# Kernel optimization log

Measured on AMD Instinct MI355X. Metric: run time of the kernel, lower is better.

The kernel has to match this reference:

```python
import jax, jax.numpy as jnp
import numpy as np

TOP_K = 8


def setup_inputs() -> dict:
    key = jax.random.key(0)
    ks = jax.random.split(key, 5)
    B, S, H, E, I = 2, 1024, 2048, 64, 768
    return {
        "hidden_states": jax.random.normal(ks[0], (B, S, H), dtype=jnp.float32),
        "router_w": jax.random.normal(ks[1], (H, E), dtype=jnp.float32) * 0.02,
        "gate_w": jax.random.normal(ks[2], (E, H, I), dtype=jnp.float32) * 0.02,
        "up_w": jax.random.normal(ks[3], (E, H, I), dtype=jnp.float32) * 0.02,
        "down_w": jax.random.normal(ks[4], (E, I, H), dtype=jnp.float32) * 0.02,
    }


def reference(hidden_states, router_w, gate_w, up_w, down_w):
    B, S, H = hidden_states.shape
    E = router_w.shape[1]
    x = hidden_states.reshape(-1, H)                      # [T, H]
    T = x.shape[0]

    router_logits = x @ router_w                           # [T, E]
    probs = jax.nn.softmax(router_logits.astype(jnp.float32), axis=-1)
    topk_w, topk_idx = jax.lax.top_k(probs, TOP_K)         # [T, K]
    topk_w = topk_w / jnp.sum(topk_w, axis=-1, keepdims=True)  # norm_topk_prob
    topk_w = topk_w.astype(x.dtype)

    # Dense combine weights: zero for non-selected experts -> same math as the
    # gather/scatter loop, jit-friendly (no data-dependent shapes).
    combine = jnp.zeros((T, E), dtype=x.dtype)
    combine = combine.at[jnp.arange(T)[:, None], topk_idx].set(topk_w)  # [T, E]

    g = jnp.einsum('th,ehi->tei', x, gate_w)               # [T, E, I]
    u = jnp.einsum('th,ehi->tei', x, up_w)                 # [T, E, I]
    h = jax.nn.silu(g) * u                                 # SwiGLU
    out = jnp.einsum('te,tei,eih->th', combine, h, down_w)  # weighted combine

    return out.reshape(B, S, H), router_logits
```

## Files before the change

kernel.cpp:

```cpp
#include <hip/hip_runtime.h>
#include <hip/hip_bf16.h>

typedef __hip_bfloat16 bf16;
typedef short s16x8 __attribute__((ext_vector_type(8)));
typedef unsigned short u16x8 __attribute__((ext_vector_type(8)));
typedef float f32x4 __attribute__((ext_vector_type(4)));

#define T_TOK 2048
#define HDIM  2048
#define NEXP  64
#define IDIM  768
#define TOPK  8
#define OUT_OFF (T_TOK * HDIM)
#define NPAIR (T_TOK * TOPK)

#define WS_TOPK_IDX  0
#define WS_TOPK_W    (64 * 1024)
#define WS_PAIR_TOK  (128 * 1024)
#define WS_SLOT_OF   (192 * 1024)
#define WS_COUNTS    (256 * 1024)
#define WS_OFFSETS   (257 * 1024)
#define WS_CURSOR    (258 * 1024)
#define WS_H         (1024 * 1024)
#define WS_PARTIAL   (WS_H + (size_t)NPAIR * IDIM * 2)
#define WS_XB        WS_PARTIAL

__device__ __forceinline__ float bf_to_f(unsigned short u) {
    return __uint_as_float(((unsigned int)u) << 16);
}
__device__ __forceinline__ unsigned short f2bf(float f) {
    unsigned int u = __float_as_uint(f);
    unsigned int r = (u + 0x7FFFu + ((u >> 16) & 1u)) >> 16;
    return (unsigned short)r;
}
__device__ __forceinline__ unsigned cvtpk(float lo, float hi) {
    unsigned r;
    asm("v_cvt_pk_bf16_f32 %0, %1, %2" : "=v"(r) : "v"(lo), "v"(hi));
    return r;
}

typedef const __attribute__((address_space(1))) unsigned int* gas_ptr;
typedef __attribute__((address_space(3))) unsigned int* las_ptr;
__device__ __forceinline__ void gload_lds16(const void* g, void* l) {
    __builtin_amdgcn_global_load_lds((gas_ptr)g, (las_ptr)l, 16, 0, 0);
}

__global__ __launch_bounds__(256) void xbf_kernel(const float* __restrict__ x,
                                                  unsigned short* __restrict__ xb) {
    int i = blockIdx.x * 256 + threadIdx.x;
    const float4* src = (const float4*)x + (size_t)i * 2;
    float4 a = src[0], b = src[1];
    u16x8 o;
    o[0] = f2bf(a.x); o[1] = f2bf(a.y); o[2] = f2bf(a.z); o[3] = f2bf(a.w);
    o[4] = f2bf(b.x); o[5] = f2bf(b.y); o[6] = f2bf(b.z); o[7] = f2bf(b.w);
    ((u16x8*)xb)[i] = o;
}

__global__ __launch_bounds__(256) void router_kernel(
    const float* __restrict__ x, const float* __restrict__ rw,
    float* __restrict__ logits) {
    int wave = threadIdx.x >> 6;
    int lane = threadIdx.x & 63;
    int t = blockIdx.x * 4 + wave;
    const float4* x4 = (const float4*)(x + (size_t)t * HDIM);
    float acc = 0.f;
    for (int h4 = 0; h4 < HDIM / 4; ++h4) {
        float4 xv = x4[h4];
        int h = h4 * 4;
        acc = fmaf(xv.x, rw[(h + 0) * NEXP + lane], acc);
        acc = fmaf(xv.y, rw[(h + 1) * NEXP + lane], acc);
        acc = fmaf(xv.z, rw[(h + 2) * NEXP + lane], acc);
        acc = fmaf(xv.w, rw[(h + 3) * NEXP + lane], acc);
    }
    logits[t * NEXP + lane] = acc;
}

__global__ __launch_bounds__(64) void topk_kernel(
    const float* __restrict__ logits, int* __restrict__ topk_idx,
    float* __restrict__ topk_w, int* __restrict__ counts) {
    int t = blockIdx.x;
    int lane = threadIdx.x;
    float lg = logits[t * NEXP + lane];
    float mx = lg;
    for (int off = 32; off; off >>= 1) mx = fmaxf(mx, __shfl_xor(mx, off));
    float ex = expf(lg - mx);
    float sum = ex;
    for (int off = 32; off; off >>= 1) sum += __shfl_xor(sum, off);
    float prob = ex / sum;

    float pr = prob;
    float myv = 0.f;
    int myidx = 0;
    float ksum = 0.f;
    for (int k = 0; k < TOPK; ++k) {
        float v = pr;
        int idx = lane;
        for (int off = 32; off; off >>= 1) {
            float ov = __shfl_xor(v, off);
            int oi = __shfl_xor(idx, off);
            if (ov > v || (ov == v && oi < idx)) { v = ov; idx = oi; }
        }
        ksum += v;
        if (lane == k) { myidx = idx; myv = v; }
        if (lane == idx) pr = -1.f;
    }
    if (lane < TOPK) {
        topk_idx[t * TOPK + lane] = myidx;
        topk_w[t * TOPK + lane] = myv / ksum;
        atomicAdd(&counts[myidx], 1);
    }
}

__global__ __launch_bounds__(64) void scan_kernel(
    const int* __restrict__ counts, int* __restrict__ offsets, int* __restrict__ cursor) {
    int lane = threadIdx.x;
    int c = counts[lane];
    int incl = c;
    for (int off = 1; off < 64; off <<= 1) {
        int tt = __shfl_up(incl, off);
        if (lane >= off) incl += tt;
    }
    offsets[lane] = incl - c;
    if (lane == 63) offsets[64] = incl;
    cursor[lane] = 0;
}

__global__ __launch_bounds__(256) void scatter_kernel(
    const int* __restrict__ topk_idx, const int* __restrict__ offsets,
    int* __restrict__ cursor, int* __restrict__ pair_token, int* __restrict__ slot_of) {
    int i = blockIdx.x * 256 + threadIdx.x;
    if (i >= NPAIR) return;
    int t = i >> 3;
    int e = topk_idx[i];
    int pos = atomicAdd(&cursor[e], 1);
    int slot = offsets[e] + pos;
    pair_token[slot] = t;
    slot_of[i] = slot;
}

#define BM   128
#define BKS  64
#define LDP  72

__global__ __launch_bounds__(256) void gateup_mfma(
    const unsigned short* __restrict__ xb, const float* __restrict__ gate_w,
    const float* __restrict__ up_w, const int* __restrict__ offsets,
    const int* __restrict__ pair_token, unsigned short* __restrict__ hbuf) {
    int e = blockIdx.x;
    int ntile = blockIdx.z;
    int off = offsets[e];
    int cnt = offsets[e + 1] - off;
    if (cnt <= 0) return;

    __shared__ unsigned short As[2][BM * BKS];
    __shared__ unsigned short Bg[2][64 * LDP];
    __shared__ unsigned short Bu[2][64 * LDP];
    __shared__ int toks[BM];

    int tid = threadIdx.x;
    int lane = tid & 63;
    int wave = tid >> 6;
    int wr = wave >> 1, wc = wave & 1;
    int l15 = lane & 15, lg4 = lane >> 4;

    int nI = tid & 15, kQ = tid >> 4;
    int n4 = nI * 4, kB = kQ * 4;
    const float* gcol = gate_w + (size_t)e * HDIM * IDIM + ntile * 64 + (size_t)kB * IDIM + n4;
    const float* ucol = up_w   + (size_t)e * HDIM * IDIM + ntile * 64 + (size_t)kB * IDIM + n4;

    for (int mt = blockIdx.y; mt * BM < cnt; mt += gridDim.y) {
        int m0 = mt * BM;
        if (tid < BM) {
            int p = m0 + tid;
            toks[tid] = pair_token[off + (p < cnt ? p : 0)];
        }
        __syncthreads();
        const unsigned short* aq[4];
        #pragma unroll
        for (int q = 0; q < 4; ++q) {
            int mloc = q * 32 + wave * 8 + (lane >> 3);
            int j2 = (lane & 7) ^ (mloc & 7);
            aq[q] = xb + (size_t)toks[mloc] * HDIM + j2 * 8;
        }
        f32x4 accg[4][2] = {};
        f32x4 accu[4][2] = {};

        #pragma unroll
        for (int q = 0; q < 4; ++q)
            gload_lds16(aq[q], &As[0][(q * 256 + wave * 64) * 8]);
        float4 G[4], U[4];
        #pragma unroll
        for (int i = 0; i < 4; ++i) {
            G[i] = *(const float4*)(gcol + (size_t)i * IDIM);
            U[i] = *(const float4*)(ucol + (size_t)i * IDIM);
        }

        for (int ks = 0; ks < HDIM / BKS; ++ks) {
            int p = ks & 1;
            #pragma unroll
            for (int j = 0; j < 4; ++j) {
                uint2 wg, wu;
                wg.x = cvtpk(((float*)&G[0])[j], ((float*)&G[1])[j]);
                wg.y = cvtpk(((float*)&G[2])[j], ((float*)&G[3])[j]);
                wu.x = cvtpk(((float*)&U[0])[j], ((float*)&U[1])[j]);
                wu.y = cvtpk(((float*)&U[2])[j], ((float*)&U[3])[j]);
                *(uint2*)&Bg[p][(n4 + j) * LDP + kB] = wg;
                *(uint2*)&Bu[p][(n4 + j) * LDP + kB] = wu;
            }
            __syncthreads();
            if (ks + 1 < HDIM / BKS) {
                int h1 = (ks + 1) * BKS;
                #pragma unroll
                for (int q = 0; q < 4; ++q)
                    gload_lds16(aq[q] + h1, &As[p ^ 1][(q * 256 + wave * 64) * 8]);
                #pragma unroll
                for (int i = 0; i < 4; ++i) {
                    G[i] = *(const float4*)(gcol + (size_t)(h1 + i) * IDIM);
                    U[i] = *(const float4*)(ucol + (size_t)(h1 + i) * IDIM);
                }
            }
            #pragma unroll
            for (int kk = 0; kk < 2; ++kk) {
                int krow = kk * 32 + lg4 * 8;
                int jk = kk * 4 + lg4;
                s16x8 a[4], bg2[2], bu2[2];
                #pragma unroll
                for (int mr = 0; mr < 4; ++mr) {
                    int r = wr * 64 + mr * 16 + l15;
                    a[mr] = *(const s16x8*)&As[p][r * 64 + ((jk ^ (r & 7)) * 8)];
                }
                #pragma unroll
                for (int nr = 0; nr < 2; ++nr) {
                    int row = wc * 32 + nr * 16 + l15;
                    bg2[nr] = *(const s16x8*)&Bg[p][row * LDP + krow];
                    bu2[nr] = *(const s16x8*)&Bu[p][row * LDP + krow];
                }
                #pragma unroll
                for (int mr = 0; mr < 4; ++mr)
                    #pragma unroll
                    for (int nr = 0; nr < 2; ++nr) {
                        accg[mr][nr] = __builtin_amdgcn_mfma_f32_16x16x32_bf16(
                            a[mr], bg2[nr], accg[mr][nr], 0, 0, 0);
                        accu[mr][nr] = __builtin_amdgcn_mfma_f32_16x16x32_bf16(
                            a[mr], bu2[nr], accu[mr][nr], 0, 0, 0);
                    }
            }
        }

        #pragma unroll
        for (int mr = 0; mr < 4; ++mr)
            #pragma unroll
            for (int nr = 0; nr < 2; ++nr) {
                int col = ntile * 64 + wc * 32 + nr * 16 + l15;
                #pragma unroll
                for (int reg = 0; reg < 4; ++reg) {
                    int r = m0 + wr * 64 + mr * 16 + lg4 * 4 + reg;
                    if (r < cnt) {
                        float g = accg[mr][nr][reg];
                        float u = accu[mr][nr][reg];
                        float hv = (g / (1.f + __expf(-g))) * u;
                        hbuf[(size_t)(off + r) * IDIM + col] = f2bf(hv);
                    }
                }
            }
    }
}

__global__ __launch_bounds__(256) void down_mfma(
    const unsigned short* __restrict__ hbuf, const float* __restrict__ down_w,
    const int* __restrict__ offsets, unsigned short* __restrict__ partial) {
    int e = blockIdx.x;
    int ntile = blockIdx.z;
    int off = offsets[e];
    int cnt = offsets[e + 1] - off;
    if (cnt <= 0) return;

    __shared__ unsigned short As[2][BM * BKS];
    __shared__ unsigned short Bd[2][128 * LDP];

    int tid = threadIdx.x;
    int lane = tid & 63;
    int wave = tid >> 6;
    int wr = wave >> 1, wc = wave & 1;
    int l15 = lane & 15, lg4 = lane >> 4;

    int nI = tid & 31, kQ0 = tid >> 5;
    int n4 = nI * 4;
    const float* dcol = down_w + (size_t)e * IDIM * HDIM + ntile * 128 + n4;

    for (int mt = blockIdx.y; mt * BM < cnt; mt += gridDim.y) {
        int m0 = mt * BM;
        const unsigned short* aq[4];
        #pragma unroll
        for (int q = 0; q < 4; ++q) {
            int mloc = q * 32 + wave * 8 + (lane >> 3);
            int row = m0 + mloc;
            if (row >= cnt) row = cnt - 1;
            int j2 = (lane & 7) ^ (mloc & 7);
            aq[q] = hbuf + (size_t)(off + row) * IDIM + j2 * 8;
        }
        f32x4 acc[4][4] = {};

        #pragma unroll
        for (int q = 0; q < 4; ++q)
            gload_lds16(aq[q], &As[0][(q * 256 + wave * 64) * 8]);
        float4 D0[4], D1[4];
        #pragma unroll
        for (int i = 0; i < 4; ++i) {
            D0[i] = *(const float4*)(dcol + (size_t)(kQ0 * 4 + i) * HDIM);
            D1[i] = *(const float4*)(dcol + (size_t)((kQ0 + 8) * 4 + i) * HDIM);
        }

        for (int ks = 0; ks < IDIM / BKS; ++ks) {
            int p = ks & 1;
            #pragma unroll
            for (int j = 0; j < 4; ++j) {
                uint2 w0, w1;
                w0.x = cvtpk(((float*)&D0[0])[j], ((float*)&D0[1])[j]);
                w0.y = cvtpk(((float*)&D0[2])[j], ((float*)&D0[3])[j]);
                w1.x = cvtpk(((float*)&D1[0])[j], ((float*)&D1[1])[j]);
                w1.y = cvtpk(((float*)&D1[2])[j], ((float*)&D1[3])[j]);
                *(uint2*)&Bd[p][(n4 + j) * LDP + kQ0 * 4] = w0;
                *(uint2*)&Bd[p][(n4 + j) * LDP + (kQ0 + 8) * 4] = w1;
            }
            __syncthreads();
            if (ks + 1 < IDIM / BKS) {
                int k1 = (ks + 1) * BKS;
                #pragma unroll
                for (int q = 0; q < 4; ++q)
                    gload_lds16(aq[q] + k1, &As[p ^ 1][(q * 256 + wave * 64) * 8]);
                #pragma unroll
                for (int i = 0; i < 4; ++i) {
                    D0[i] = *(const float4*)(dcol + (size_t)(k1 + kQ0 * 4 + i) * HDIM);
                    D1[i] = *(const float4*)(dcol + (size_t)(k1 + (kQ0 + 8) * 4 + i) * HDIM);
                }
            }
            #pragma unroll
            for (int kk = 0; kk < 2; ++kk) {
                int krow = kk * 32 + lg4 * 8;
                int jk = kk * 4 + lg4;
                s16x8 a[4], b[4];
                #pragma unroll
                for (int mr = 0; mr < 4; ++mr) {
                    int r = wr * 64 + mr * 16 + l15;
                    a[mr] = *(const s16x8*)&As[p][r * 64 + ((jk ^ (r & 7)) * 8)];
                }
                #pragma unroll
                for (int nr = 0; nr < 4; ++nr) {
                    int row = wc * 64 + nr * 16 + l15;
                    b[nr] = *(const s16x8*)&Bd[p][row * LDP + krow];
                }
                #pragma unroll
                for (int mr = 0; mr < 4; ++mr)
                    #pragma unroll
                    for (int nr = 0; nr < 4; ++nr)
                        acc[mr][nr] = __builtin_amdgcn_mfma_f32_16x16x32_bf16(
                            a[mr], b[nr], acc[mr][nr], 0, 0, 0);
            }
        }

        #pragma unroll
        for (int mr = 0; mr < 4; ++mr)
            #pragma unroll
            for (int nr = 0; nr < 4; ++nr) {
                int col = ntile * 128 + wc * 64 + nr * 16 + l15;
                #pragma unroll
                for (int reg = 0; reg < 4; ++reg) {
                    int r = m0 + wr * 64 + mr * 16 + lg4 * 4 + reg;
                    if (r < cnt)
                        partial[(size_t)(off + r) * HDIM + col] = f2bf(acc[mr][nr][reg]);
                }
            }
        __syncthreads();
    }
}

__global__ __launch_bounds__(256) void reduce_kernel(
    const unsigned short* __restrict__ partial, const int* __restrict__ slot_of,
    const float* __restrict__ topk_w, float* __restrict__ out) {
    int t = blockIdx.x;
    int j8 = threadIdx.x * 8;
    __shared__ int ss[8];
    __shared__ float sw[8];
    if (threadIdx.x < 8) {
        ss[threadIdx.x] = slot_of[t * TOPK + threadIdx.x];
        sw[threadIdx.x] = topk_w[t * TOPK + threadIdx.x];
    }
    __syncthreads();
    float acc[8] = {};
    #pragma unroll
    for (int k = 0; k < TOPK; ++k) {
        u16x8 v = *(const u16x8*)&partial[(size_t)ss[k] * HDIM + j8];
        float w = sw[k];
        #pragma unroll
        for (int i = 0; i < 8; ++i)
            acc[i] = fmaf(w, bf_to_f((unsigned short)v[i]), acc[i]);
    }
    float4 o0 = {acc[0], acc[1], acc[2], acc[3]};
    float4 o1 = {acc[4], acc[5], acc[6], acc[7]};
    *(float4*)&out[(size_t)t * HDIM + j8] = o0;
    *(float4*)&out[(size_t)t * HDIM + j8 + 4] = o1;
}

extern "C" void kernel_launch(void* const* d_in, const int* in_sizes, int n_in,
                              void* d_out, int out_size, void* d_ws, size_t ws_size,
                              hipStream_t stream) {
    const float* x  = (const float*)d_in[0];
    const float* rw = (const float*)d_in[1];
    const float* gw = (const float*)d_in[2];
    const float* uw = (const float*)d_in[3];
    const float* dw = (const float*)d_in[4];
    float* out = (float*)d_out;
    float* logits = out + OUT_OFF;

    char* ws = (char*)d_ws;
    int*   topk_idx   = (int*)(ws + WS_TOPK_IDX);
    float* topk_w     = (float*)(ws + WS_TOPK_W);
    int*   pair_token = (int*)(ws + WS_PAIR_TOK);
    int*   slot_of    = (int*)(ws + WS_SLOT_OF);
    int*   counts     = (int*)(ws + WS_COUNTS);
    int*   offsets    = (int*)(ws + WS_OFFSETS);
    int*   cursor     = (int*)(ws + WS_CURSOR);
    unsigned short* hbuf    = (unsigned short*)(ws + WS_H);
    unsigned short* partial = (unsigned short*)(ws + WS_PARTIAL);
    unsigned short* xb      = (unsigned short*)(ws + WS_XB);

    hipMemsetAsync(counts, 0, NEXP * sizeof(int), stream);
    xbf_kernel<<<T_TOK * HDIM / (256 * 8), 256, 0, stream>>>(x, xb);
    router_kernel<<<T_TOK / 4, 256, 0, stream>>>(x, rw, logits);
    topk_kernel<<<T_TOK, 64, 0, stream>>>(logits, topk_idx, topk_w, counts);
    scan_kernel<<<1, 64, 0, stream>>>(counts, offsets, cursor);
    scatter_kernel<<<NPAIR / 256, 256, 0, stream>>>(topk_idx, offsets, cursor, pair_token, slot_of);
    gateup_mfma<<<dim3(NEXP, 4, IDIM / 64), 256, 0, stream>>>(xb, gw, uw, offsets, pair_token, hbuf);
    down_mfma<<<dim3(NEXP, 4, HDIM / 128), 256, 0, stream>>>(hbuf, dw, offsets, partial);
    reduce_kernel<<<dim3(T_TOK, 1), 256, 0, stream>>>(partial, slot_of, topk_w, out);
}
```

Before: 726.8 us.

## Swizzle weight LDS tiles with 16-byte stores and halve M-tile grid

Replaces the padded (LDP=72) weight tiles in both expert GEMMs with unpadded tiles that use an XOR swizzle. Each thread now loads float2 pairs across 8 k-rows and writes packed bf16 as 16-byte uint4 stores, where before it wrote 8-byte stores. This is meant to cut LDS bank conflicts and store instruction count. The grid y dimension drops from 4 to 2, so each block loops over more M tiles, which trades parallelism for weight reuse in cache. A sync is added at the end of the gate/up M-tile loop to protect the toks buffer.

```diff
diff --git a/kernel.cpp b/kernel.cpp
--- a/kernel.cpp
+++ b/kernel.cpp
@@ -140,7 +140,6 @@
 
 #define BM   128
 #define BKS  64
-#define LDP  72
 
 __global__ __launch_bounds__(256) void gateup_mfma(
     const unsigned short* __restrict__ xb, const float* __restrict__ gate_w,
@@ -153,8 +152,8 @@
     if (cnt <= 0) return;
 
     __shared__ unsigned short As[2][BM * BKS];
-    __shared__ unsigned short Bg[2][64 * LDP];
-    __shared__ unsigned short Bu[2][64 * LDP];
+    __shared__ unsigned short Bg[2][64 * BKS];
+    __shared__ unsigned short Bu[2][64 * BKS];
     __shared__ int toks[BM];
 
     int tid = threadIdx.x;
@@ -163,10 +162,12 @@
     int wr = wave >> 1, wc = wave & 1;
     int l15 = lane & 15, lg4 = lane >> 4;
 
-    int nI = tid & 15, kQ = tid >> 4;
-    int n4 = nI * 4, kB = kQ * 4;
-    const float* gcol = gate_w + (size_t)e * HDIM * IDIM + ntile * 64 + (size_t)kB * IDIM + n4;
-    const float* ucol = up_w   + (size_t)e * HDIM * IDIM + ntile * 64 + (size_t)kB * IDIM + n4;
+    int nI2 = tid & 31;
+    int kC  = tid >> 5;
+    int bn0 = nI2 * 2;
+    int wslot = (kC ^ (nI2 & 7)) * 8;
+    const float* gp = gate_w + (size_t)e * HDIM * IDIM + (size_t)(kC * 8) * IDIM + ntile * 64 + bn0;
+    const float* upp = up_w  + (size_t)e * HDIM * IDIM + (size_t)(kC * 8) * IDIM + ntile * 64 + bn0;
 
     for (int mt = blockIdx.y; mt * BM < cnt; mt += gridDim.y) {
         int m0 = mt * BM;
@@ -188,24 +189,29 @@
         #pragma unroll
         for (int q = 0; q < 4; ++q)
             gload_lds16(aq[q], &As[0][(q * 256 + wave * 64) * 8]);
-        float4 G[4], U[4];
-        #pragma unroll
-        for (int i = 0; i < 4; ++i) {
-            G[i] = *(const float4*)(gcol + (size_t)i * IDIM);
-            U[i] = *(const float4*)(ucol + (size_t)i * IDIM);
+        float2 G2[8], U2[8];
+        #pragma unroll
+        for (int i = 0; i < 8; ++i) {
+            G2[i] = *(const float2*)(gp + (size_t)i * IDIM);
+            U2[i] = *(const float2*)(upp + (size_t)i * IDIM);
         }
 
         for (int ks = 0; ks < HDIM / BKS; ++ks) {
             int p = ks & 1;
-            #pragma unroll
-            for (int j = 0; j < 4; ++j) {
-                uint2 wg, wu;
-                wg.x = cvtpk(((float*)&G[0])[j], ((float*)&G[1])[j]);
-                wg.y = cvtpk(((float*)&G[2])[j], ((float*)&G[3])[j]);
-                wu.x = cvtpk(((float*)&U[0])[j], ((float*)&U[1])[j]);
-                wu.y = cvtpk(((float*)&U[2])[j], ((float*)&U[3])[j]);
-                *(uint2*)&Bg[p][(n4 + j) * LDP + kB] = wg;
-                *(uint2*)&Bu[p][(n4 + j) * LDP + kB] = wu;
+            {
+                uint4 wg0, wg1, wu0, wu1;
+                wg0.x = cvtpk(G2[0].x, G2[1].x); wg0.y = cvtpk(G2[2].x, G2[3].x);
+                wg0.z = cvtpk(G2[4].x, G2[5].x); wg0.w = cvtpk(G2[6].x, G2[7].x);
+                wg1.x = cvtpk(G2[0].y, G2[1].y); wg1.y = cvtpk(G2[2].y, G2[3].y);
+                wg1.z = cvtpk(G2[4].y, G2[5].y); wg1.w = cvtpk(G2[6].y, G2[7].y);
+                wu0.x = cvtpk(U2[0].x, U2[1].x); wu0.y = cvtpk(U2[2].x, U2[3].x);
+                wu0.z = cvtpk(U2[4].x, U2[5].x); wu0.w = cvtpk(U2[6].x, U2[7].x);
+                wu1.x = cvtpk(U2[0].y, U2[1].y); wu1.y = cvtpk(U2[2].y, U2[3].y);
+                wu1.z = cvtpk(U2[4].y, U2[5].y); wu1.w = cvtpk(U2[6].y, U2[7].y);
+                *(uint4*)&Bg[p][bn0 * BKS + wslot] = wg0;
+                *(uint4*)&Bg[p][(bn0 + 1) * BKS + wslot] = wg1;
+                *(uint4*)&Bu[p][bn0 * BKS + wslot] = wu0;
+                *(uint4*)&Bu[p][(bn0 + 1) * BKS + wslot] = wu1;
             }
             __syncthreads();
             if (ks + 1 < HDIM / BKS) {
@@ -214,26 +220,26 @@
                 for (int q = 0; q < 4; ++q)
                     gload_lds16(aq[q] + h1, &As[p ^ 1][(q * 256 + wave * 64) * 8]);
                 #pragma unroll
-                for (int i = 0; i < 4; ++i) {
-                    G[i] = *(const float4*)(gcol + (size_t)(h1 + i) * IDIM);
-                    U[i] = *(const float4*)(ucol + (size_t)(h1 + i) * IDIM);
+                for (int i = 0; i < 8; ++i) {
+                    G2[i] = *(const float2*)(gp + (size_t)(h1 + i) * IDIM);
+                    U2[i] = *(const float2*)(upp + (size_t)(h1 + i) * IDIM);
                 }
             }
             #pragma unroll
             for (int kk = 0; kk < 2; ++kk) {
-                int krow = kk * 32 + lg4 * 8;
                 int jk = kk * 4 + lg4;
                 s16x8 a[4], bg2[2], bu2[2];
                 #pragma unroll
                 for (int mr = 0; mr < 4; ++mr) {
                     int r = wr * 64 + mr * 16 + l15;
-                    a[mr] = *(const s16x8*)&As[p][r * 64 + ((jk ^ (r & 7)) * 8)];
+                    a[mr] = *(const s16x8*)&As[p][r * BKS + ((jk ^ (r & 7)) * 8)];
                 }
                 #pragma unroll
                 for (int nr = 0; nr < 2; ++nr) {
                     int row = wc * 32 + nr * 16 + l15;
-                    bg2[nr] = *(const s16x8*)&Bg[p][row * LDP + krow];
-                    bu2[nr] = *(const s16x8*)&Bu[p][row * LDP + krow];
+                    int slot = (jk ^ ((row >> 1) & 7)) * 8;
+                    bg2[nr] = *(const s16x8*)&Bg[p][row * BKS + slot];
+                    bu2[nr] = *(const s16x8*)&Bu[p][row * BKS + slot];
                 }
                 #pragma unroll
                 for (int mr = 0; mr < 4; ++mr)
@@ -263,6 +269,7 @@
                     }
                 }
             }
+        __syncthreads();
     }
 }
 
@@ -276,7 +283,7 @@
     if (cnt <= 0) return;
 
     __shared__ unsigned short As[2][BM * BKS];
-    __shared__ unsigned short Bd[2][128 * LDP];
+    __shared__ unsigned short Bd[2][128 * BKS];
 
     int tid = threadIdx.x;
     int lane = tid & 63;
@@ -284,9 +291,12 @@
     int wr = wave >> 1, wc = wave & 1;
     int l15 = lane & 15, lg4 = lane >> 4;
 
-    int nI = tid & 31, kQ0 = tid >> 5;
-    int n4 = nI * 4;
-    const float* dcol = down_w + (size_t)e * IDIM * HDIM + ntile * 128 + n4;
+    int nI2 = tid & 63;
+    int kC0 = tid >> 6;
+    int bn0 = nI2 * 2;
+    int wslotA = (kC0 ^ (nI2 & 7)) * 8;
+    int wslotB = ((kC0 + 4) ^ (nI2 & 7)) * 8;
+    const float* dp = down_w + (size_t)e * IDIM * HDIM + ntile * 128 + bn0;
 
     for (int mt = blockIdx.y; mt * BM < cnt; mt += gridDim.y) {
         int m0 = mt * BM;
@@ -304,24 +314,29 @@
         #pragma unroll
         for (int q = 0; q < 4; ++q)
             gload_lds16(aq[q], &As[0][(q * 256 + wave * 64) * 8]);
-        float4 D0[4], D1[4];
-        #pragma unroll
-        for (int i = 0; i < 4; ++i) {
-            D0[i] = *(const float4*)(dcol + (size_t)(kQ0 * 4 + i) * HDIM);
-            D1[i] = *(const float4*)(dcol + (size_t)((kQ0 + 8) * 4 + i) * HDIM);
+        float2 Da[8], Db[8];
+        #pragma unroll
+        for (int i = 0; i < 8; ++i) {
+            Da[i] = *(const float2*)(dp + (size_t)(kC0 * 8 + i) * HDIM);
+            Db[i] = *(const float2*)(dp + (size_t)(kC0 * 8 + 32 + i) * HDIM);
         }
 
         for (int ks = 0; ks < IDIM / BKS; ++ks) {
             int p = ks & 1;
-            #pragma unroll
-            for (int j = 0; j < 4; ++j) {
-                uint2 w0, w1;
-                w0.x = cvtpk(((float*)&D0[0])[j], ((float*)&D0[1])[j]);
-                w0.y = cvtpk(((float*)&D0[2])[j], ((float*)&D0[3])[j]);
-                w1.x = cvtpk(((float*)&D1[0])[j], ((float*)&D1[1])[j]);
-                w1.y = cvtpk(((float*)&D1[2])[j], ((float*)&D1[3])[j]);
-                *(uint2*)&Bd[p][(n4 + j) * LDP + kQ0 * 4] = w0;
-                *(uint2*)&Bd[p][(n4 + j) * LDP + (kQ0 + 8) * 4] = w1;
+            {
+                uint4 w0, w1, w2, w3;
+                w0.x = cvtpk(Da[0].x, Da[1].x); w0.y = cvtpk(Da[2].x, Da[3].x);
+                w0.z = cvtpk(Da[4].x, Da[5].x); w0.w = cvtpk(Da[6].x, Da[7].x);
+                w1.x = cvtpk(Da[0].y, Da[1].y); w1.y = cvtpk(Da[2].y, Da[3].y);
+                w1.z = cvtpk(Da[4].y, Da[5].y); w1.w = cvtpk(Da[6].y, Da[7].y);
+                w2.x = cvtpk(Db[0].x, Db[1].x); w2.y = cvtpk(Db[2].x, Db[3].x);
+                w2.z = cvtpk(Db[4].x, Db[5].x); w2.w = cvtpk(Db[6].x, Db[7].x);
+                w3.x = cvtpk(Db[0].y, Db[1].y); w3.y = cvtpk(Db[2].y, Db[3].y);
+                w3.z = cvtpk(Db[4].y, Db[5].y); w3.w = cvtpk(Db[6].y, Db[7].y);
+                *(uint4*)&Bd[p][bn0 * BKS + wslotA] = w0;
+                *(uint4*)&Bd[p][(bn0 + 1) * BKS + wslotA] = w1;
+                *(uint4*)&Bd[p][bn0 * BKS + wslotB] = w2;
+                *(uint4*)&Bd[p][(bn0 + 1) * BKS + wslotB] = w3;
             }
             __syncthreads();
             if (ks + 1 < IDIM / BKS) {
@@ -330,25 +345,25 @@
                 for (int q = 0; q < 4; ++q)
                     gload_lds16(aq[q] + k1, &As[p ^ 1][(q * 256 + wave * 64) * 8]);
                 #pragma unroll
-                for (int i = 0; i < 4; ++i) {
-                    D0[i] = *(const float4*)(dcol + (size_t)(k1 + kQ0 * 4 + i) * HDIM);
-                    D1[i] = *(const float4*)(dcol + (size_t)(k1 + (kQ0 + 8) * 4 + i) * HDIM);
+                for (int i = 0; i < 8; ++i) {
+                    Da[i] = *(const float2*)(dp + (size_t)(k1 + kC0 * 8 + i) * HDIM);
+                    Db[i] = *(const float2*)(dp + (size_t)(k1 + kC0 * 8 + 32 + i) * HDIM);
                 }
             }
             #pragma unroll
             for (int kk = 0; kk < 2; ++kk) {
-                int krow = kk * 32 + lg4 * 8;
                 int jk = kk * 4 + lg4;
                 s16x8 a[4], b[4];
                 #pragma unroll
                 for (int mr = 0; mr < 4; ++mr) {
                     int r = wr * 64 + mr * 16 + l15;
-                    a[mr] = *(const s16x8*)&As[p][r * 64 + ((jk ^ (r & 7)) * 8)];
+                    a[mr] = *(const s16x8*)&As[p][r * BKS + ((jk ^ (r & 7)) * 8)];
                 }
                 #pragma unroll
                 for (int nr = 0; nr < 4; ++nr) {
                     int row = wc * 64 + nr * 16 + l15;
-                    b[nr] = *(const s16x8*)&Bd[p][row * LDP + krow];
+                    int slot = (jk ^ ((row >> 1) & 7)) * 8;
+                    b[nr] = *(const s16x8*)&Bd[p][row * BKS + slot];
                 }
                 #pragma unroll
                 for (int mr = 0; mr < 4; ++mr)
@@ -431,7 +446,7 @@
     topk_kernel<<<T_TOK, 64, 0, stream>>>(logits, topk_idx, topk_w, counts);
     scan_kernel<<<1, 64, 0, stream>>>(counts, offsets, cursor);
     scatter_kernel<<<NPAIR / 256, 256, 0, stream>>>(topk_idx, offsets, cursor, pair_token, slot_of);
-    gateup_mfma<<<dim3(NEXP, 4, IDIM / 64), 256, 0, stream>>>(xb, gw, uw, offsets, pair_token, hbuf);
-    down_mfma<<<dim3(NEXP, 4, HDIM / 128), 256, 0, stream>>>(hbuf, dw, offsets, partial);
+    gateup_mfma<<<dim3(NEXP, 2, IDIM / 64), 256, 0, stream>>>(xb, gw, uw, offsets, pair_token, hbuf);
+    down_mfma<<<dim3(NEXP, 2, HDIM / 128), 256, 0, stream>>>(hbuf, dw, offsets, partial);
     reduce_kernel<<<dim3(T_TOK, 1), 256, 0, stream>>>(partial, slot_of, topk_w, out);
 }
```

Result: slower. 872.4 us (+20.0%).

## Double block size to 512 threads and swizzle B tiles in LDS for MoE GEMMs

Applied to the files above, without the earlier changes.

Both expert GEMM kernels now run with 512 threads (8 waves in a 2x4 grid) instead of 256, so each wave owns a smaller output tile and holds fewer accumulators. Weight tiles are loaded as float2 pairs, converted to bf16 and written as 16-byte vectors into an XOR-swizzled LDS layout with no padding. Gate and up weights share one buffer, with half the threads loading each matrix. The aim is more waves to hide global-load latency and fewer LDS bank conflicts. The trade-off is less A-fragment reuse per wave and an extra barrier at the end of each m-tile.

```diff
diff --git a/kernel.cpp b/kernel.cpp
--- a/kernel.cpp
+++ b/kernel.cpp
@@ -140,9 +140,8 @@
 
 #define BM   128
 #define BKS  64
-#define LDP  72
-
-__global__ __launch_bounds__(256) void gateup_mfma(
+
+__global__ __launch_bounds__(512, 4) void gateup_mfma(
     const unsigned short* __restrict__ xb, const float* __restrict__ gate_w,
     const float* __restrict__ up_w, const int* __restrict__ offsets,
     const int* __restrict__ pair_token, unsigned short* __restrict__ hbuf) {
@@ -153,20 +152,22 @@
     if (cnt <= 0) return;
 
     __shared__ unsigned short As[2][BM * BKS];
-    __shared__ unsigned short Bg[2][64 * LDP];
-    __shared__ unsigned short Bu[2][64 * LDP];
+    __shared__ unsigned short Bgu[2][BM * BKS];
     __shared__ int toks[BM];
 
     int tid = threadIdx.x;
     int lane = tid & 63;
     int wave = tid >> 6;
-    int wr = wave >> 1, wc = wave & 1;
+    int wr = wave >> 2, wc = wave & 3;
     int l15 = lane & 15, lg4 = lane >> 4;
 
-    int nI = tid & 15, kQ = tid >> 4;
-    int n4 = nI * 4, kB = kQ * 4;
-    const float* gcol = gate_w + (size_t)e * HDIM * IDIM + ntile * 64 + (size_t)kB * IDIM + n4;
-    const float* ucol = up_w   + (size_t)e * HDIM * IDIM + ntile * 64 + (size_t)kB * IDIM + n4;
+    int mat = tid >> 8;
+    int t8 = tid & 255;
+    int nI2 = t8 & 31, kC = t8 >> 5;
+    int brow0 = mat * 64 + nI2 * 2;
+    int bslot = (kC ^ (nI2 & 7)) * 8;
+    const float* bsrc = (mat ? up_w : gate_w) + (size_t)e * HDIM * IDIM
+                        + (size_t)(kC * 8) * IDIM + ntile * 64 + nI2 * 2;
 
     for (int mt = blockIdx.y; mt * BM < cnt; mt += gridDim.y) {
         int m0 = mt * BM;
@@ -175,98 +176,84 @@
             toks[tid] = pair_token[off + (p < cnt ? p : 0)];
         }
         __syncthreads();
-        const unsigned short* aq[4];
-        #pragma unroll
-        for (int q = 0; q < 4; ++q) {
-            int mloc = q * 32 + wave * 8 + (lane >> 3);
-            int j2 = (lane & 7) ^ (mloc & 7);
-            aq[q] = xb + (size_t)toks[mloc] * HDIM + j2 * 8;
-        }
-        f32x4 accg[4][2] = {};
-        f32x4 accu[4][2] = {};
-
-        #pragma unroll
-        for (int q = 0; q < 4; ++q)
-            gload_lds16(aq[q], &As[0][(q * 256 + wave * 64) * 8]);
-        float4 G[4], U[4];
-        #pragma unroll
-        for (int i = 0; i < 4; ++i) {
-            G[i] = *(const float4*)(gcol + (size_t)i * IDIM);
-            U[i] = *(const float4*)(ucol + (size_t)i * IDIM);
-        }
+        const unsigned short* aq[2];
+        #pragma unroll
+        for (int q = 0; q < 2; ++q) {
+            int row = q * 64 + (tid >> 3);
+            aq[q] = xb + (size_t)toks[row] * HDIM + (((tid & 7) ^ (row & 7)) * 8);
+        }
+        f32x4 accg[4] = {};
+        f32x4 accu[4] = {};
+
+        #pragma unroll
+        for (int q = 0; q < 2; ++q)
+            gload_lds16(aq[q], &As[0][(q * 512 + tid) * 8]);
+        float2 Bv[8];
+        #pragma unroll
+        for (int i = 0; i < 8; ++i)
+            Bv[i] = *(const float2*)(bsrc + (size_t)i * IDIM);
 
         for (int ks = 0; ks < HDIM / BKS; ++ks) {
             int p = ks & 1;
-            #pragma unroll
-            for (int j = 0; j < 4; ++j) {
-                uint2 wg, wu;
-                wg.x = cvtpk(((float*)&G[0])[j], ((float*)&G[1])[j]);
-                wg.y = cvtpk(((float*)&G[2])[j], ((float*)&G[3])[j]);
-                wu.x = cvtpk(((float*)&U[0])[j], ((float*)&U[1])[j]);
-                wu.y = cvtpk(((float*)&U[2])[j], ((float*)&U[3])[j]);
-                *(uint2*)&Bg[p][(n4 + j) * LDP + kB] = wg;
-                *(uint2*)&Bu[p][(n4 + j) * LDP + kB] = wu;
+            {
+                uint4 w0, w1;
+                w0.x = cvtpk(Bv[0].x, Bv[1].x); w0.y = cvtpk(Bv[2].x, Bv[3].x);
+                w0.z = cvtpk(Bv[4].x, Bv[5].x); w0.w = cvtpk(Bv[6].x, Bv[7].x);
+                w1.x = cvtpk(Bv[0].y, Bv[1].y); w1.y = cvtpk(Bv[2].y, Bv[3].y);
+                w1.z = cvtpk(Bv[4].y, Bv[5].y); w1.w = cvtpk(Bv[6].y, Bv[7].y);
+                *(uint4*)&Bgu[p][brow0 * BKS + bslot] = w0;
+                *(uint4*)&Bgu[p][(brow0 + 1) * BKS + bslot] = w1;
             }
             __syncthreads();
             if (ks + 1 < HDIM / BKS) {
                 int h1 = (ks + 1) * BKS;
                 #pragma unroll
-                for (int q = 0; q < 4; ++q)
-                    gload_lds16(aq[q] + h1, &As[p ^ 1][(q * 256 + wave * 64) * 8]);
-                #pragma unroll
-                for (int i = 0; i < 4; ++i) {
-                    G[i] = *(const float4*)(gcol + (size_t)(h1 + i) * IDIM);
-                    U[i] = *(const float4*)(ucol + (size_t)(h1 + i) * IDIM);
-                }
+                for (int q = 0; q < 2; ++q)
+                    gload_lds16(aq[q] + h1, &As[p ^ 1][(q * 512 + tid) * 8]);
+                #pragma unroll
+                for (int i = 0; i < 8; ++i)
+                    Bv[i] = *(const float2*)(bsrc + (size_t)(h1 + i) * IDIM);
             }
             #pragma unroll
             for (int kk = 0; kk < 2; ++kk) {
-                int krow = kk * 32 + lg4 * 8;
                 int jk = kk * 4 + lg4;
-                s16x8 a[4], bg2[2], bu2[2];
+                s16x8 a[4], bg, bu;
                 #pragma unroll
                 for (int mr = 0; mr < 4; ++mr) {
                     int r = wr * 64 + mr * 16 + l15;
-                    a[mr] = *(const s16x8*)&As[p][r * 64 + ((jk ^ (r & 7)) * 8)];
-                }
-                #pragma unroll
-                for (int nr = 0; nr < 2; ++nr) {
-                    int row = wc * 32 + nr * 16 + l15;
-                    bg2[nr] = *(const s16x8*)&Bg[p][row * LDP + krow];
-                    bu2[nr] = *(const s16x8*)&Bu[p][row * LDP + krow];
-                }
-                #pragma unroll
-                for (int mr = 0; mr < 4; ++mr)
-                    #pragma unroll
-                    for (int nr = 0; nr < 2; ++nr) {
-                        accg[mr][nr] = __builtin_amdgcn_mfma_f32_16x16x32_bf16(
-                            a[mr], bg2[nr], accg[mr][nr], 0, 0, 0);
-                        accu[mr][nr] = __builtin_amdgcn_mfma_f32_16x16x32_bf16(
-                            a[mr], bu2[nr], accu[mr][nr], 0, 0, 0);
-                    }
-            }
-        }
-
-        #pragma unroll
-        for (int mr = 0; mr < 4; ++mr)
+                    a[mr] = *(const s16x8*)&As[p][r * BKS + ((jk ^ (r & 7)) * 8)];
+                }
+                int rg = wc * 16 + l15;
+                int ru = 64 + rg;
+                bg = *(const s16x8*)&Bgu[p][rg * BKS + ((jk ^ ((rg >> 1) & 7)) * 8)];
+                bu = *(const s16x8*)&Bgu[p][ru * BKS + ((jk ^ ((ru >> 1) & 7)) * 8)];
+                #pragma unroll
+                for (int mr = 0; mr < 4; ++mr) {
+                    accg[mr] = __builtin_amdgcn_mfma_f32_16x16x32_bf16(a[mr], bg, accg[mr], 0, 0, 0);
+                    accu[mr] = __builtin_amdgcn_mfma_f32_16x16x32_bf16(a[mr], bu, accu[mr], 0, 0, 0);
+                }
+            }
+        }
+
+        int col = ntile * 64 + wc * 16 + l15;
+        #pragma unroll
+        for (int mr = 0; mr < 4; ++mr) {
             #pragma unroll
-            for (int nr = 0; nr < 2; ++nr) {
-                int col = ntile * 64 + wc * 32 + nr * 16 + l15;
-                #pragma unroll
-                for (int reg = 0; reg < 4; ++reg) {
-                    int r = m0 + wr * 64 + mr * 16 + lg4 * 4 + reg;
-                    if (r < cnt) {
-                        float g = accg[mr][nr][reg];
-                        float u = accu[mr][nr][reg];
-                        float hv = (g / (1.f + __expf(-g))) * u;
-                        hbuf[(size_t)(off + r) * IDIM + col] = f2bf(hv);
-                    }
-                }
-            }
-    }
-}
-
-__global__ __launch_bounds__(256) void down_mfma(
+            for (int reg = 0; reg < 4; ++reg) {
+                int r = m0 + wr * 64 + mr * 16 + lg4 * 4 + reg;
+                if (r < cnt) {
+                    float g = accg[mr][reg];
+                    float u = accu[mr][reg];
+                    float hv = (g / (1.f + __expf(-g))) * u;
+                    hbuf[(size_t)(off + r) * IDIM + col] = f2bf(hv);
+                }
+            }
+        }
+        __syncthreads();
+    }
+}
+
+__global__ __launch_bounds__(512, 4) void down_mfma(
     const unsigned short* __restrict__ hbuf, const float* __restrict__ down_w,
     const int* __restrict__ offsets, unsigned short* __restrict__ partial) {
     int e = blockIdx.x;
@@ -276,84 +263,79 @@
     if (cnt <= 0) return;
 
     __shared__ unsigned short As[2][BM * BKS];
-    __shared__ unsigned short Bd[2][128 * LDP];
+    __shared__ unsigned short Bd[2][BM * BKS];
 
     int tid = threadIdx.x;
     int lane = tid & 63;
     int wave = tid >> 6;
-    int wr = wave >> 1, wc = wave & 1;
+    int wr = wave >> 2, wc = wave & 3;
     int l15 = lane & 15, lg4 = lane >> 4;
 
-    int nI = tid & 31, kQ0 = tid >> 5;
-    int n4 = nI * 4;
-    const float* dcol = down_w + (size_t)e * IDIM * HDIM + ntile * 128 + n4;
+    int nI2 = tid & 63, kC = tid >> 6;
+    int brow0 = nI2 * 2;
+    int bslot = (kC ^ (nI2 & 7)) * 8;
+    const float* bsrc = down_w + (size_t)e * IDIM * HDIM
+                        + (size_t)(kC * 8) * HDIM + ntile * 128 + nI2 * 2;
 
     for (int mt = blockIdx.y; mt * BM < cnt; mt += gridDim.y) {
         int m0 = mt * BM;
-        const unsigned short* aq[4];
-        #pragma unroll
-        for (int q = 0; q < 4; ++q) {
-            int mloc = q * 32 + wave * 8 + (lane >> 3);
-            int row = m0 + mloc;
-            if (row >= cnt) row = cnt - 1;
-            int j2 = (lane & 7) ^ (mloc & 7);
-            aq[q] = hbuf + (size_t)(off + row) * IDIM + j2 * 8;
-        }
-        f32x4 acc[4][4] = {};
-
-        #pragma unroll
-        for (int q = 0; q < 4; ++q)
-            gload_lds16(aq[q], &As[0][(q * 256 + wave * 64) * 8]);
-        float4 D0[4], D1[4];
-        #pragma unroll
-        for (int i = 0; i < 4; ++i) {
-            D0[i] = *(const float4*)(dcol + (size_t)(kQ0 * 4 + i) * HDIM);
-            D1[i] = *(const float4*)(dcol + (size_t)((kQ0 + 8) * 4 + i) * HDIM);
-        }
+        const unsigned short* aq[2];
+        #pragma unroll
+        for (int q = 0; q < 2; ++q) {
+            int row = q * 64 + (tid >> 3);
+            int rr = m0 + row;
+            if (rr >= cnt) rr = cnt - 1;
+            aq[q] = hbuf + (size_t)(off + rr) * IDIM + (((tid & 7) ^ (row & 7)) * 8);
+        }
+        f32x4 acc[4][2] = {};
+
+        #pragma unroll
+        for (int q = 0; q < 2; ++q)
+            gload_lds16(aq[q], &As[0][(q * 512 + tid) * 8]);
+        float2 Bv[8];
+        #pragma unroll
+        for (int i = 0; i < 8; ++i)
+            Bv[i] = *(const float2*)(bsrc + (size_t)i * HDIM);
 
         for (int ks = 0; ks < IDIM / BKS; ++ks) {
             int p = ks & 1;
-            #pragma unroll
-            for (int j = 0; j < 4; ++j) {
-                uint2 w0, w1;
-                w0.x = cvtpk(((float*)&D0[0])[j], ((float*)&D0[1])[j]);
-                w0.y = cvtpk(((float*)&D0[2])[j], ((float*)&D0[3])[j]);
-                w1.x = cvtpk(((float*)&D1[0])[j], ((float*)&D1[1])[j]);
-                w1.y = cvtpk(((float*)&D1[2])[j], ((float*)&D1[3])[j]);
-                *(uint2*)&Bd[p][(n4 + j) * LDP + kQ0 * 4] = w0;
-                *(uint2*)&Bd[p][(n4 + j) * LDP + (kQ0 + 8) * 4] = w1;
+            {
+                uint4 w0, w1;
+                w0.x = cvtpk(Bv[0].x, Bv[1].x); w0.y = cvtpk(Bv[2].x, Bv[3].x);
+                w0.z = cvtpk(Bv[4].x, Bv[5].x); w0.w = cvtpk(Bv[6].x, Bv[7].x);
+                w1.x = cvtpk(Bv[0].y, Bv[1].y); w1.y = cvtpk(Bv[2].y, Bv[3].y);
+                w1.z = cvtpk(Bv[4].y, Bv[5].y); w1.w = cvtpk(Bv[6].y, Bv[7].y);
+                *(uint4*)&Bd[p][brow0 * BKS + bslot] = w0;
+                *(uint4*)&Bd[p][(brow0 + 1) * BKS + bslot] = w1;
             }
             __syncthreads();
             if (ks + 1 < IDIM / BKS) {
                 int k1 = (ks + 1) * BKS;
                 #pragma unroll
-                for (int q = 0; q < 4; ++q)
-                    gload_lds16(aq[q] + k1, &As[p ^ 1][(q * 256 + wave * 64) * 8]);
-                #pragma unroll
-                for (int i = 0; i < 4; ++i) {
-                    D0[i] = *(const float4*)(dcol + (size_t)(k1 + kQ0 * 4 + i) * HDIM);
-                    D1[i] = *(const float4*)(dcol + (size_t)(k1 + (kQ0 + 8) * 4 + i) * HDIM);
-                }
+                for (int q = 0; q < 2; ++q)
+                    gload_lds16(aq[q] + k1, &As[p ^ 1][(q * 512 + tid) * 8]);
+                #pragma unroll
+                for (int i = 0; i < 8; ++i)
+                    Bv[i] = *(const float2*)(bsrc + (size_t)(k1 + i) * HDIM);
             }
             #pragma unroll
             for (int kk = 0; kk < 2; ++kk) {
-                int krow = kk * 32 + lg4 * 8;
                 int jk = kk * 4 + lg4;
-                s16x8 a[4], b[4];
+                s16x8 a[4], b[2];
                 #pragma unroll
                 for (int mr = 0; mr < 4; ++mr) {
                     int r = wr * 64 + mr * 16 + l15;
-                    a[mr] = *(const s16x8*)&As[p][r * 64 + ((jk ^ (r & 7)) * 8)];
-                }
-                #pragma unroll
-                for (int nr = 0; nr < 4; ++nr) {
-                    int row = wc * 64 + nr * 16 + l15;
-                    b[nr] = *(const s16x8*)&Bd[p][row * LDP + krow];
+                    a[mr] = *(const s16x8*)&As[p][r * BKS + ((jk ^ (r & 7)) * 8)];
+                }
+                #pragma unroll
+                for (int nr = 0; nr < 2; ++nr) {
+                    int row = wc * 32 + nr * 16 + l15;
+                    b[nr] = *(const s16x8*)&Bd[p][row * BKS + ((jk ^ ((row >> 1) & 7)) * 8)];
                 }
                 #pragma unroll
                 for (int mr = 0; mr < 4; ++mr)
                     #pragma unroll
-                    for (int nr = 0; nr < 4; ++nr)
+                    for (int nr = 0; nr < 2; ++nr)
                         acc[mr][nr] = __builtin_amdgcn_mfma_f32_16x16x32_bf16(
                             a[mr], b[nr], acc[mr][nr], 0, 0, 0);
             }
@@ -362,8 +344,8 @@
         #pragma unroll
         for (int mr = 0; mr < 4; ++mr)
             #pragma unroll
-            for (int nr = 0; nr < 4; ++nr) {
-                int col = ntile * 128 + wc * 64 + nr * 16 + l15;
+            for (int nr = 0; nr < 2; ++nr) {
+                int col = ntile * 128 + wc * 32 + nr * 16 + l15;
                 #pragma unroll
                 for (int reg = 0; reg < 4; ++reg) {
                     int r = m0 + wr * 64 + mr * 16 + lg4 * 4 + reg;
@@ -431,7 +413,7 @@
     topk_kernel<<<T_TOK, 64, 0, stream>>>(logits, topk_idx, topk_w, counts);
     scan_kernel<<<1, 64, 0, stream>>>(counts, offsets, cursor);
     scatter_kernel<<<NPAIR / 256, 256, 0, stream>>>(topk_idx, offsets, cursor, pair_token, slot_of);
-    gateup_mfma<<<dim3(NEXP, 4, IDIM / 64), 256, 0, stream>>>(xb, gw, uw, offsets, pair_token, hbuf);
-    down_mfma<<<dim3(NEXP, 4, HDIM / 128), 256, 0, stream>>>(hbuf, dw, offsets, partial);
+    gateup_mfma<<<dim3(NEXP, 4, IDIM / 64), 512, 0, stream>>>(xb, gw, uw, offsets, pair_token, hbuf);
+    down_mfma<<<dim3(NEXP, 4, HDIM / 128), 512, 0, stream>>>(hbuf, dw, offsets, partial);
     reduce_kernel<<<dim3(T_TOK, 1), 256, 0, stream>>>(partial, slot_of, topk_w, out);
 }
```

Result: faster. 674.1 us (-7.3%).
